# Performance work log

Hardware: AMD Instinct MI355X
Metric: run time of the kernel (lower is better)

Reference implementation:

```python
import jax, jax.numpy as jnp
import numpy as np
from jax import lax

B, N_PARAMS, N_LAYERS = 8, 4, 5
CIN, COUT, K, MID = 64, 64, 3, 64
H, W = 256, 256
LAYER_IDX = 2
PAD = (K - 1) // 2  # 'preserve' padding, stride=1


def setup_inputs() -> dict:
    key = jax.random.key(0)
    ks = jax.random.split(key, 16)
    s = 0.002  # embedder init scale (xavier_normal_(x, 0.002) ~ tiny weights)
    inp = {
        "x": jax.random.normal(ks[0], (B, CIN, H, W), jnp.float32),
        "h": jax.random.normal(ks[1], (B, N_PARAMS), jnp.float32),
        "index": jnp.zeros((N_LAYERS,), jnp.float32).at[LAYER_IDX].set(1.0),
        "conv_weight": jax.random.normal(ks[2], (COUT, CIN, K, K), jnp.float32) * 0.05,
        "conv_bias": jax.random.normal(ks[3], (COUT,), jnp.float32) * 0.05,
        "W_wp": jax.random.normal(ks[4], (MID * CIN, N_PARAMS), jnp.float32) * s,
        "b_wp": jnp.zeros((MID * CIN,), jnp.float32),
        "W_wi": jax.random.normal(ks[5], (MID * CIN, N_LAYERS), jnp.float32) * s,
        "b_wi": jnp.zeros((MID * CIN,), jnp.float32),
        "W_we": jax.random.normal(ks[6], (COUT * K * K, MID), jnp.float32) * s,
        "b_we": jnp.zeros((COUT * K * K,), jnp.float32),
        "W_bp": jax.random.normal(ks[7], (COUT, N_PARAMS), jnp.float32) * s,
        "b_bp": jnp.zeros((COUT,), jnp.float32),
        "W_bi": jax.random.normal(ks[8], (COUT, N_LAYERS), jnp.float32) * s,
        "b_bi": jnp.zeros((COUT,), jnp.float32),
    }
    return inp


def _embed(h, index, W_wp, b_wp, W_wi, b_wi, W_we, b_we, W_bp, b_bp, W_bi, b_bi):
    # fc_w_param(h) + fc_w_index(index): (B, mid*in)
    w = h @ W_wp.T + b_wp + index @ W_wi.T + b_wi
    w = w.reshape(-1, CIN, MID)                      # (B, in, mid)
    w = w @ W_we.T + b_we                            # (B, in, out*k*k)
    w = w.reshape(-1, CIN, COUT, K, K).swapaxes(1, 2)  # (B, out, in, k, k)
    b = h @ W_bp.T + b_bp + index @ W_bi.T + b_bi    # (B, out)
    return w, b


def reference(x, h, index, conv_weight, conv_bias,
              W_wp, b_wp, W_wi, b_wi, W_we, b_we,
              W_bp, b_bp, W_bi, b_bi):
    dw, db = _embed(h, index, W_wp, b_wp, W_wi, b_wi, W_we, b_we,
                    W_bp, b_bp, W_bi, b_bi)
    weights = conv_weight[None] + dw           # (B, out, in, k, k)
    bias = conv_bias[None] + db                # (B, out)

    def conv_one(xi, wi):
        # xi: (in, H, W), wi: (out, in, k, k) -> (out, H, W)
        y = lax.conv_general_dilated(
            xi[None], wi, window_strides=(1, 1),
            padding=((PAD, PAD), (PAD, PAD)),
            dimension_numbers=("NCHW", "OIHW", "NCHW"))
        return y[0]

    y = jax.vmap(conv_one)(x, weights)         # per-sample weights == batch-as-groups conv
    return y + bias[:, :, None, None]
```

## Files before the change

kernel.cpp:

```cpp
#include <hip/hip_runtime.h>
#include <hip/hip_bf16.h>

typedef short  short8  __attribute__((ext_vector_type(8)));
typedef float  f32x16  __attribute__((ext_vector_type(16)));
typedef unsigned short ushort_t;

#define B_    8
#define CIN_  64
#define COUT_ 64
#define MID_  64
#define HH    256
#define WW    256
#define NP_   4
#define NL_   5

#define TR 8
#define TC 32
#define NJT 8
#define SR 10
#define SCC 34
#define SLAB_U32 (SR*8*SCC*4)
#define W_SHORTS (9*8*COUT_*8)
#define NSTG 22

__global__ __launch_bounds__(256)
void build_weights(const float* __restrict__ h, const float* __restrict__ index,
                   const float* __restrict__ conv_weight,
                   const float* __restrict__ W_wp, const float* __restrict__ b_wp,
                   const float* __restrict__ W_wi, const float* __restrict__ b_wi,
                   const float* __restrict__ W_we, const float* __restrict__ b_we,
                   ushort_t* __restrict__ wsW) {
    const int bb  = blockIdx.x / 9;
    const int ch  = blockIdx.x - bb * 9;
    const int tid = threadIdx.x;

    __shared__ float pre_s[64 * 66];
    __shared__ float chunk_s[64 * 64];

    float hv[NP_], iv[NL_];
#pragma unroll
    for (int p = 0; p < NP_; ++p) hv[p] = h[bb * NP_ + p];
#pragma unroll
    for (int l = 0; l < NL_; ++l) iv[l] = index[l];

#pragma unroll
    for (int k = 0; k < 16; ++k) {
        const int m = tid + k * 256;
        float a = b_wp[m] + b_wi[m];
#pragma unroll
        for (int p = 0; p < NP_; ++p) a += hv[p] * W_wp[m * NP_ + p];
#pragma unroll
        for (int l = 0; l < NL_; ++l) a += iv[l] * W_wi[m * NL_ + l];
        pre_s[(m >> 6) * 66 + (m & 63)] = a;
    }
#pragma unroll
    for (int k = 0; k < 16; ++k) {
        const int f = tid + k * 256;
        chunk_s[f] = W_we[ch * 4096 + f];
    }
    __syncthreads();

    const int ci = tid & 63;
    const int g  = tid >> 6;
    float acc[16];
#pragma unroll
    for (int u = 0; u < 16; ++u) acc[u] = 0.f;

#pragma unroll
    for (int mid = 0; mid < 64; mid += 2) {
        const float2 pv = *(const float2*)&pre_s[ci * 66 + mid];
#pragma unroll
        for (int u = 0; u < 16; ++u) {
            const float2 wv = *(const float2*)&chunk_s[(g + 4 * u) * 64 + mid];
            acc[u] += pv.x * wv.x + pv.y * wv.y;
        }
    }

#pragma unroll
    for (int u = 0; u < 16; ++u) {
        const int o9 = ch * 64 + g + 4 * u;
        const int co = o9 / 9;
        const int r  = o9 - co * 9;
        const float val = acc[u] + b_we[o9] + conv_weight[(co * CIN_ + ci) * 9 + r];
        __hip_bfloat16 hb = __float2bfloat16(val);
        ushort_t bits; __builtin_memcpy(&bits, &hb, 2);
        wsW[(((bb * 9 + r) * 8 + (ci >> 3)) * COUT_ + co) * 8 + (ci & 7)] = bits;
    }
}

__device__ __forceinline__ void load_tile(const float* __restrict__ xb, int i0, int j0,
                                          int tid, unsigned (&vals)[NSTG]) {
#pragma unroll
    for (int k = 0; k < NSTG; ++k) {
        const int s = tid + k * 512;
        unsigned v = 0u;
        if (s < SLAB_U32) {
            const int p  = s & 3;
            const int t2 = s >> 2;
            const int c  = t2 % SCC;
            const int t3 = t2 / SCC;
            const int g  = t3 & 7;
            const int r  = t3 >> 3;
            const int gr = i0 - 1 + r;
            const int gc = j0 - 1 + c;
            const int ci = g * 8 + p * 2;
            const bool ok = ((unsigned)gr < (unsigned)HH) && ((unsigned)gc < (unsigned)WW);
            const float* px = xb + ci * (HH * WW) + (ok ? (gr * WW + gc) : 0);
            float f0 = px[0];
            float f1 = px[HH * WW];
            if (!ok) { f0 = 0.f; f1 = 0.f; }
            const __hip_bfloat162 h2 = __float22bfloat162_rn(make_float2(f0, f1));
            __builtin_memcpy(&v, &h2, 4);
        }
        vals[k] = v;
    }
}

__global__ __launch_bounds__(512, 2)
void hyperconv(const float* __restrict__ x, const ushort_t* __restrict__ wsW,
               const float* __restrict__ conv_bias,
               const float* __restrict__ h, const float* __restrict__ index,
               const float* __restrict__ W_bp, const float* __restrict__ b_bp,
               const float* __restrict__ W_bi, const float* __restrict__ b_bi,
               float* __restrict__ out) {
    __shared__ __align__(16) ushort_t Wl[W_SHORTS];
    __shared__ __align__(16) unsigned Slab[SLAB_U32];
    __shared__ float biasl[COUT_];

    const int tid   = threadIdx.x;
    const int bb    = blockIdx.x >> 5;
    const int strip = blockIdx.x & 31;
    const int i0    = strip * TR;
    const float* xb = x + bb * CIN_ * HH * WW;

    unsigned vals[NSTG];
    load_tile(xb, i0, 0, tid, vals);

    {
        const uint4* src = (const uint4*)(wsW + bb * W_SHORTS);
        uint4* dst = (uint4*)Wl;
        for (int i = tid; i < W_SHORTS / 8; i += 512) dst[i] = src[i];
    }
    if (tid < COUT_) {
        const int co = tid;
        float a = conv_bias[co] + b_bp[co] + b_bi[co];
#pragma unroll
        for (int p = 0; p < NP_; ++p) a += h[bb * NP_ + p] * W_bp[co * NP_ + p];
#pragma unroll
        for (int l = 0; l < NL_; ++l) a += index[l] * W_bi[co * NL_ + l];
        biasl[co] = a;
    }

    const int lane = tid & 63;
    const int wv   = tid >> 6;
    const int n    = lane & 31;
    const int hl   = lane >> 5;

    for (int jt = 0; jt < NJT; ++jt) {
        __syncthreads();
#pragma unroll
        for (int k = 0; k < NSTG; ++k) {
            const int s = tid + k * 512;
            if (s < SLAB_U32) Slab[s] = vals[k];
        }
        if (jt + 1 < NJT) load_tile(xb, i0, (jt + 1) * TC, tid, vals);
        __syncthreads();

        f32x16 a0 = {}, a1 = {};
        const ushort_t* sl = (const ushort_t*)Slab;
#pragma unroll
        for (int kh = 0; kh < 3; ++kh)
#pragma unroll
            for (int kw = 0; kw < 3; ++kw) {
                const int khkw = kh * 3 + kw;
#pragma unroll
                for (int kk = 0; kk < 4; ++kk) {
                    const int gA = khkw * 8 + 2 * kk + hl;
                    const short8 A0 = *(const short8*)&Wl[(gA * 64 + n) * 8];
                    const short8 A1 = *(const short8*)&Wl[(gA * 64 + n + 32) * 8];
                    const int gB = ((wv + kh) * 8 + 2 * kk + hl) * SCC + (n + kw);
                    const short8 Bf = *(const short8*)&sl[gB * 8];
                    a0 = __builtin_amdgcn_mfma_f32_32x32x16_bf16(A0, Bf, a0, 0, 0, 0);
                    a1 = __builtin_amdgcn_mfma_f32_32x32x16_bf16(A1, Bf, a1, 0, 0, 0);
                }
            }

        const int j0 = jt * TC;
        float* op = out + (size_t)(bb * COUT_) * (HH * WW) + (i0 + wv) * WW + j0 + n;
#pragma unroll
        for (int r = 0; r < 16; ++r) {
            const int co = (r & 3) + 8 * (r >> 2) + 4 * hl;
            op[co * (HH * WW)] = a0[r] + biasl[co];
        }
#pragma unroll
        for (int r = 0; r < 16; ++r) {
            const int co = (r & 3) + 8 * (r >> 2) + 4 * hl + 32;
            op[co * (HH * WW)] = a1[r] + biasl[co];
        }
    }
}

extern "C" void kernel_launch(void* const* d_in, const int* in_sizes, int n_in,
                              void* d_out, int out_size, void* d_ws, size_t ws_size,
                              hipStream_t stream) {
    const float* x           = (const float*)d_in[0];
    const float* h           = (const float*)d_in[1];
    const float* index       = (const float*)d_in[2];
    const float* conv_weight = (const float*)d_in[3];
    const float* conv_bias   = (const float*)d_in[4];
    const float* W_wp        = (const float*)d_in[5];
    const float* b_wp        = (const float*)d_in[6];
    const float* W_wi        = (const float*)d_in[7];
    const float* b_wi        = (const float*)d_in[8];
    const float* W_we        = (const float*)d_in[9];
    const float* b_we        = (const float*)d_in[10];
    const float* W_bp        = (const float*)d_in[11];
    const float* b_bp        = (const float*)d_in[12];
    const float* W_bi        = (const float*)d_in[13];
    const float* b_bi        = (const float*)d_in[14];

    float* out = (float*)d_out;
    ushort_t* wsW = (ushort_t*)d_ws;

    build_weights<<<72, 256, 0, stream>>>(
        h, index, conv_weight, W_wp, b_wp, W_wi, b_wi, W_we, b_we, wsW);

    hyperconv<<<256, 512, 0, stream>>>(
        x, wsW, conv_bias, h, index, W_bp, b_bp, W_bi, b_bi, out);
}
```

Baseline: 325.5 us.

## Vectorize halo tile loads with precomputed offsets and lighter barriers

The input slab loader is rebuilt. Each thread now loads float2 pairs of columns, using per-thread offsets and store indices computed once before the tile loop, instead of per-element divides and bounds checks on every tile. A separate clamped edge loader handles the first and last column tiles, and zero-masking for padding is applied when the values are written to shared memory. The slab row is widened to 36 columns for alignment. The __syncthreads calls are replaced by raw s_barrier with sched_barriers and an explicit lgkmcnt wait, which adds register pressure and a risk of subtle ordering bugs.

Result: slower. 335.9 us (+3.2%).

```diff
diff --git a/kernel.cpp b/kernel.cpp
--- a/kernel.cpp
+++ b/kernel.cpp
@@ -18,10 +18,12 @@
 #define TC 32
 #define NJT 8
 #define SR 10
-#define SCC 34
+#define SCC 36
 #define SLAB_U32 (SR*8*SCC*4)
 #define W_SHORTS (9*8*COUT_*8)
-#define NSTG 22
+#define NUNITS (SR*8*4*18)
+#define NU 12
+#define LASTU (NUNITS - 512*(NU-1))
 
 __global__ __launch_bounds__(256)
 void build_weights(const float* __restrict__ h, const float* __restrict__ index,
@@ -88,31 +90,32 @@
     }
 }
 
-__device__ __forceinline__ void load_tile(const float* __restrict__ xb, int i0, int j0,
-                                          int tid, unsigned (&vals)[NSTG]) {
-#pragma unroll
-    for (int k = 0; k < NSTG; ++k) {
-        const int s = tid + k * 512;
-        unsigned v = 0u;
-        if (s < SLAB_U32) {
-            const int p  = s & 3;
-            const int t2 = s >> 2;
-            const int c  = t2 % SCC;
-            const int t3 = t2 / SCC;
-            const int g  = t3 & 7;
-            const int r  = t3 >> 3;
-            const int gr = i0 - 1 + r;
-            const int gc = j0 - 1 + c;
-            const int ci = g * 8 + p * 2;
-            const bool ok = ((unsigned)gr < (unsigned)HH) && ((unsigned)gc < (unsigned)WW);
-            const float* px = xb + ci * (HH * WW) + (ok ? (gr * WW + gc) : 0);
-            float f0 = px[0];
-            float f1 = px[HH * WW];
-            if (!ok) { f0 = 0.f; f1 = 0.f; }
-            const __hip_bfloat162 h2 = __float22bfloat162_rn(make_float2(f0, f1));
-            __builtin_memcpy(&v, &h2, 4);
-        }
-        vals[k] = v;
+
+__device__ __forceinline__ void load_fast(const float* __restrict__ xb,
+                                          const int (&rel)[NU], int j0,
+                                          float2 (&va)[NU], float2 (&vb)[NU]) {
+#pragma unroll
+    for (int k = 0; k < NU; ++k) {
+        const float* p0 = xb + (rel[k] + j0);
+        va[k] = *(const float2*)p0;
+        vb[k] = *(const float2*)(p0 + HH * WW);
+    }
+}
+
+__device__ __forceinline__ void load_edge(const float* __restrict__ xb,
+                                          const int (&rel)[NU], const int (&cc2)[NU], int j0,
+                                          float2 (&va)[NU], float2 (&vb)[NU]) {
+#pragma unroll
+    for (int k = 0; k < NU; ++k) {
+        const int base = rel[k] - cc2[k];
+        const int gc0  = j0 + cc2[k];
+        const int c0 = gc0 < 0 ? 0 : (gc0 > WW - 1 ? WW - 1 : gc0);
+        const int g1 = gc0 + 1;
+        const int c1 = g1 < 0 ? 0 : (g1 > WW - 1 ? WW - 1 : g1);
+        va[k].x = xb[base + c0];
+        va[k].y = xb[base + c1];
+        vb[k].x = xb[base + HH * WW + c0];
+        vb[k].y = xb[base + HH * WW + c1];
     }
 }
 
@@ -133,13 +136,34 @@
     const int i0    = strip * TR;
     const float* xb = x + bb * CIN_ * HH * WW;
 
-    unsigned vals[NSTG];
-    load_tile(xb, i0, 0, tid, vals);
+    int rel[NU], cc2[NU], sidx[NU];
+    unsigned rmask = 0u;
+#pragma unroll
+    for (int k = 0; k < NU; ++k) {
+        int u = tid + k * 512;
+        const bool uok = (u < NUNITS);
+        if (!uok) u = NUNITS - 1;
+        const int cp = u % 18;
+        const int t  = u / 18;
+        const int p  = t & 3;
+        const int rg = t >> 2;
+        const int g  = rg & 7;
+        const int r  = rg >> 3;
+        const int gr = i0 - 1 + r;
+        const int grc = gr < 0 ? 0 : (gr > HH - 1 ? HH - 1 : gr);
+        const int ci = g * 8 + 2 * p;
+        cc2[k]  = 2 * cp - 2;
+        rel[k]  = ci * (HH * WW) + grc * WW + cc2[k];
+        sidx[k] = (rg * SCC + 2 * cp) * 4 + p;
+        if (uok && (unsigned)gr < (unsigned)HH) rmask |= 1u << k;
+    }
 
     {
         const uint4* src = (const uint4*)(wsW + bb * W_SHORTS);
         uint4* dst = (uint4*)Wl;
-        for (int i = tid; i < W_SHORTS / 8; i += 512) dst[i] = src[i];
+#pragma unroll
+        for (int i = 0; i < (W_SHORTS / 8) / 512; ++i)
+            dst[tid + i * 512] = src[tid + i * 512];
     }
     if (tid < COUT_) {
         const int co = tid;
@@ -150,6 +174,9 @@
         for (int l = 0; l < NL_; ++l) a += index[l] * W_bi[co * NL_ + l];
         biasl[co] = a;
     }
+
+    float2 va[NU], vb[NU];
+    load_edge(xb, rel, cc2, 0, va, vb);
 
     const int lane = tid & 63;
     const int wv   = tid >> 6;
@@ -157,14 +184,41 @@
     const int hl   = lane >> 5;
 
     for (int jt = 0; jt < NJT; ++jt) {
-        __syncthreads();
-#pragma unroll
-        for (int k = 0; k < NSTG; ++k) {
-            const int s = tid + k * 512;
-            if (s < SLAB_U32) Slab[s] = vals[k];
-        }
-        if (jt + 1 < NJT) load_tile(xb, i0, (jt + 1) * TC, tid, vals);
-        __syncthreads();
+        const int j0 = jt * TC;
+        __builtin_amdgcn_sched_barrier(0);
+        __builtin_amdgcn_s_barrier();
+        __builtin_amdgcn_sched_barrier(0);
+
+#pragma unroll
+        for (int k = 0; k < NU; ++k) {
+            if (k == NU - 1 && tid >= LASTU) continue;
+            const bool rok = (rmask >> k) & 1u;
+            const int gc0 = j0 + cc2[k];
+            const bool ok0 = rok && ((unsigned)gc0 < (unsigned)WW);
+            const bool ok1 = rok && ((unsigned)(gc0 + 1) < (unsigned)WW);
+            const float ax = ok0 ? va[k].x : 0.f;
+            const float bx = ok0 ? vb[k].x : 0.f;
+            const float ay = ok1 ? va[k].y : 0.f;
+            const float by = ok1 ? vb[k].y : 0.f;
+            const __hip_bfloat162 lo2 = __float22bfloat162_rn(make_float2(ax, bx));
+            const __hip_bfloat162 hi2 = __float22bfloat162_rn(make_float2(ay, by));
+            unsigned ulo, uhi;
+            __builtin_memcpy(&ulo, &lo2, 4);
+            __builtin_memcpy(&uhi, &hi2, 4);
+            Slab[sidx[k]]     = ulo;
+            Slab[sidx[k] + 4] = uhi;
+        }
+
+        if (jt + 1 < NJT) {
+            if (jt + 1 == NJT - 1) load_edge(xb, rel, cc2, (jt + 1) * TC, va, vb);
+            else                   load_fast(xb, rel, (jt + 1) * TC, va, vb);
+        }
+
+        __builtin_amdgcn_sched_barrier(0);
+        asm volatile("s_waitcnt lgkmcnt(0)" ::: "memory");
+        __builtin_amdgcn_sched_barrier(0);
+        __builtin_amdgcn_s_barrier();
+        __builtin_amdgcn_sched_barrier(0);
 
         f32x16 a0 = {}, a1 = {};
         const ushort_t* sl = (const ushort_t*)Slab;
@@ -178,14 +232,13 @@
                     const int gA = khkw * 8 + 2 * kk + hl;
                     const short8 A0 = *(const short8*)&Wl[(gA * 64 + n) * 8];
                     const short8 A1 = *(const short8*)&Wl[(gA * 64 + n + 32) * 8];
-                    const int gB = ((wv + kh) * 8 + 2 * kk + hl) * SCC + (n + kw);
+                    const int gB = ((wv + kh) * 8 + 2 * kk + hl) * SCC + (n + kw + 1);
                     const short8 Bf = *(const short8*)&sl[gB * 8];
                     a0 = __builtin_amdgcn_mfma_f32_32x32x16_bf16(A0, Bf, a0, 0, 0, 0);
                     a1 = __builtin_amdgcn_mfma_f32_32x32x16_bf16(A1, Bf, a1, 0, 0, 0);
                 }
             }
 
-        const int j0 = jt * TC;
         float* op = out + (size_t)(bb * COUT_) * (HH * WW) + (i0 + wv) * WW + j0 + n;
 #pragma unroll
         for (int r = 0; r < 16; ++r) {
```

## Split output channels across two blocks to double grid and raise occupancy

Applied to the files above, without the earlier changes.

Each block now computes only half of the 64 output channels. This doubles the grid to 512 blocks, halves the weight LDS footprint and the accumulator registers, and raises launch bounds to 4 waves-per-SIMD occupancy. Block indexing is also reordered so adjacent blocks handle different batches for the same strip. The cost is that each input tile is loaded and converted to bf16 twice, once per half, which doubles the global x traffic.

Result: slower. 439.2 us (+34.9%).

```diff
diff --git a/kernel.cpp b/kernel.cpp
--- a/kernel.cpp
+++ b/kernel.cpp
@@ -21,6 +21,7 @@
 #define SCC 34
 #define SLAB_U32 (SR*8*SCC*4)
 #define W_SHORTS (9*8*COUT_*8)
+#define WL_SHORTS (9*8*32*8)
 #define NSTG 22
 
 __global__ __launch_bounds__(256)
@@ -116,20 +117,23 @@
     }
 }
 
-__global__ __launch_bounds__(512, 2)
+__global__ __launch_bounds__(512, 4)
 void hyperconv(const float* __restrict__ x, const ushort_t* __restrict__ wsW,
                const float* __restrict__ conv_bias,
                const float* __restrict__ h, const float* __restrict__ index,
                const float* __restrict__ W_bp, const float* __restrict__ b_bp,
                const float* __restrict__ W_bi, const float* __restrict__ b_bi,
                float* __restrict__ out) {
-    __shared__ __align__(16) ushort_t Wl[W_SHORTS];
+    __shared__ __align__(16) ushort_t Wl[WL_SHORTS];
     __shared__ __align__(16) unsigned Slab[SLAB_U32];
-    __shared__ float biasl[COUT_];
-
-    const int tid   = threadIdx.x;
-    const int bb    = blockIdx.x >> 5;
-    const int strip = blockIdx.x & 31;
+    __shared__ float biasl[32];
+
+    const int tid  = threadIdx.x;
+    const int p    = blockIdx.x;
+    const int half  = p >> 8;
+    const int rest  = p & 255;
+    const int bb    = rest & 7;
+    const int strip = rest >> 3;
     const int i0    = strip * TR;
     const float* xb = x + bb * CIN_ * HH * WW;
 
@@ -139,16 +143,24 @@
     {
         const uint4* src = (const uint4*)(wsW + bb * W_SHORTS);
         uint4* dst = (uint4*)Wl;
-        for (int i = tid; i < W_SHORTS / 8; i += 512) dst[i] = src[i];
-    }
-    if (tid < COUT_) {
-        const int co = tid;
+#pragma unroll
+        for (int k = 0; k < 5; ++k) {
+            const int idx = tid + k * 512;
+            if (idx < (WL_SHORTS / 8)) {
+                const int row = idx >> 5;
+                const int off = idx & 31;
+                dst[idx] = src[row * 64 + half * 32 + off];
+            }
+        }
+    }
+    if (tid < 32) {
+        const int co = half * 32 + tid;
         float a = conv_bias[co] + b_bp[co] + b_bi[co];
 #pragma unroll
-        for (int p = 0; p < NP_; ++p) a += h[bb * NP_ + p] * W_bp[co * NP_ + p];
+        for (int q = 0; q < NP_; ++q) a += h[bb * NP_ + q] * W_bp[co * NP_ + q];
 #pragma unroll
         for (int l = 0; l < NL_; ++l) a += index[l] * W_bi[co * NL_ + l];
-        biasl[co] = a;
+        biasl[tid] = a;
     }
 
     const int lane = tid & 63;
@@ -166,7 +178,7 @@
         if (jt + 1 < NJT) load_tile(xb, i0, (jt + 1) * TC, tid, vals);
         __syncthreads();
 
-        f32x16 a0 = {}, a1 = {};
+        f32x16 a0 = {};
         const ushort_t* sl = (const ushort_t*)Slab;
 #pragma unroll
         for (int kh = 0; kh < 3; ++kh)
@@ -176,26 +188,20 @@
 #pragma unroll
                 for (int kk = 0; kk < 4; ++kk) {
                     const int gA = khkw * 8 + 2 * kk + hl;
-                    const short8 A0 = *(const short8*)&Wl[(gA * 64 + n) * 8];
-                    const short8 A1 = *(const short8*)&Wl[(gA * 64 + n + 32) * 8];
+                    const short8 A0 = *(const short8*)&Wl[(gA * 32 + n) * 8];
                     const int gB = ((wv + kh) * 8 + 2 * kk + hl) * SCC + (n + kw);
                     const short8 Bf = *(const short8*)&sl[gB * 8];
                     a0 = __builtin_amdgcn_mfma_f32_32x32x16_bf16(A0, Bf, a0, 0, 0, 0);
-                    a1 = __builtin_amdgcn_mfma_f32_32x32x16_bf16(A1, Bf, a1, 0, 0, 0);
                 }
             }
 
         const int j0 = jt * TC;
-        float* op = out + (size_t)(bb * COUT_) * (HH * WW) + (i0 + wv) * WW + j0 + n;
+        float* op = out + (size_t)(bb * COUT_ + half * 32) * (HH * WW)
+                  + (i0 + wv) * WW + j0 + n;
 #pragma unroll
         for (int r = 0; r < 16; ++r) {
-            const int co = (r & 3) + 8 * (r >> 2) + 4 * hl;
-            op[co * (HH * WW)] = a0[r] + biasl[co];
-        }
-#pragma unroll
-        for (int r = 0; r < 16; ++r) {
-            const int co = (r & 3) + 8 * (r >> 2) + 4 * hl + 32;
-            op[co * (HH * WW)] = a1[r] + biasl[co];
+            const int col = (r & 3) + 8 * (r >> 2) + 4 * hl;
+            op[col * (HH * WW)] = a0[r] + biasl[col];
         }
     }
 }
@@ -225,6 +231,6 @@
     build_weights<<<72, 256, 0, stream>>>(
         h, index, conv_weight, W_wp, b_wp, W_wi, b_wi, W_we, b_we, wsW);
 
-    hyperconv<<<256, 512, 0, stream>>>(
+    hyperconv<<<512, 512, 0, stream>>>(
         x, wsW, conv_bias, h, index, W_bp, b_bp, W_bi, b_bi, out);
 }
```
